# Performance work log

Hardware: AMD Instinct MI355X
Metric: run time of the kernel (lower is better)

The kernel has to match this reference:

```python
import jax, jax.numpy as jnp
import numpy as np

N_HEAD = 16
LORA_RANK = 16
ROPE_BASE = 10000.0


def _rope_cos_sin(T, D, dtype):
    # GPT-NeoX style rotate-half RoPE tables, shape [T, D]
    inv_freq = 1.0 / (ROPE_BASE ** (jnp.arange(0, D, 2, dtype=jnp.float32) / D))
    t = jnp.arange(T, dtype=jnp.float32)
    freqs = t[:, None] * inv_freq[None, :]          # [T, D/2]
    emb = jnp.concatenate([freqs, freqs], axis=-1)   # [T, D]
    return jnp.cos(emb).astype(dtype), jnp.sin(emb).astype(dtype)


def _rotate_half(x):
    x1, x2 = jnp.split(x, 2, axis=-1)
    return jnp.concatenate([-x2, x1], axis=-1)


def _apply_rope(q, k, cos, sin):
    # q,k: [B,H,T,D]; cos,sin: [T,D]
    c = cos[None, None, :, :]
    s = sin[None, None, :, :]
    return q * c + _rotate_half(q) * s, k * c + _rotate_half(k) * s


def setup_inputs() -> dict:
    key = jax.random.key(0)
    ks = jax.random.split(key, 6)
    B, T, C = 4, 1024, 2048
    r = LORA_RANK
    sc = 1.0 / np.sqrt(C)
    return {
        "x": jax.random.normal(ks[0], (B, T, C), jnp.float32),
        "qkvo_delta": jax.random.normal(ks[1], (B, 8 * r, C), jnp.float32) * 0.02,
        "Wq": jax.random.normal(ks[2], (C, C), jnp.float32) * sc,
        "Wk": jax.random.normal(ks[3], (C, C), jnp.float32) * sc,
        "Wv": jax.random.normal(ks[4], (C, C), jnp.float32) * sc,
        "Wo": jax.random.normal(ks[5], (C, C), jnp.float32) * sc,
    }


def reference(x, qkvo_delta, Wq, Wk, Wv, Wo):
    B, T, C = x.shape
    H = N_HEAD
    D = C // H

    # split LoRA deltas: each [B, r, C]
    dqA, dqB, dkA, dkB, dvA, dvB, doA, doB = jnp.split(qkvo_delta, 8, axis=1)

    def merged(W, dB, dA):
        # W [out,in] + dB^T @ dA -> [B, out, in]
        return W[None] + jnp.einsum('bro,bri->boi', dB, dA)

    def proj(inp, Wm):
        # inp @ Wm^T (per-batch merged weight)
        return jnp.einsum('bti,boi->bto', inp, Wm)

    q = proj(x, merged(Wq, dqB, dqA))
    k = proj(x, merged(Wk, dkB, dkA))
    v = proj(x, merged(Wv, dvB, dvA))

    # [B,T,C] -> [B,H,T,D]
    def heads(t):
        return t.reshape(B, T, H, D).transpose(0, 2, 1, 3)

    q, k, v = heads(q), heads(k), heads(v)

    cos, sin = _rope_cos_sin(T, D, x.dtype)
    q, k = _apply_rope(q, k, cos, sin)

    # full (non-causal) SDPA, matching is_causal=False in the source
    scale = 1.0 / np.sqrt(D)
    scores = jnp.einsum('bhtd,bhsd->bhts', q, k) * scale
    attn = jax.nn.softmax(scores, axis=-1)
    y = jnp.einsum('bhts,bhsd->bhtd', attn, v)

    y = y.transpose(0, 2, 1, 3).reshape(B, T, C)
    out = proj(y, merged(Wo, doB, doA))
    return out
```

## Files before the change

kernel.cpp:

```cpp
#include <hip/hip_runtime.h>
#include <cstdint>
#include <cstddef>

typedef __attribute__((ext_vector_type(8))) __bf16 bf8_t;
typedef __attribute__((ext_vector_type(8))) short s8_t;
typedef __attribute__((ext_vector_type(4))) short s4_t;
typedef __attribute__((ext_vector_type(4))) float f4_t;

__device__ __forceinline__ float bf2f(unsigned short h) {
  union { unsigned u; float f; } v; v.u = (unsigned)h << 16; return v.f;
}
__device__ __forceinline__ unsigned short f2bf(float f) {
  union { float f; unsigned u; } v; v.f = f;
  return (unsigned short)((v.u + 0x7FFFu + ((v.u >> 16) & 1u)) >> 16);
}

#define GL16(gp, lp) __builtin_amdgcn_global_load_lds( \
    (__attribute__((address_space(1))) void*)(gp),     \
    (__attribute__((address_space(3))) void*)(lp), 16, 0, 0)

__global__ void k_f32_to_bf16(const float* __restrict__ in,
                              unsigned short* __restrict__ out, int n4) {
  int i = blockIdx.x * blockDim.x + threadIdx.x;
  if (i >= n4) return;
  float4 v = reinterpret_cast<const float4*>(in)[i];
  s4_t o;
  o.x = (short)f2bf(v.x); o.y = (short)f2bf(v.y);
  o.z = (short)f2bf(v.z); o.w = (short)f2bf(v.w);
  reinterpret_cast<s4_t*>(out)[i] = o;
}

struct P4 { const float* in[4]; unsigned short* out[4]; };
__global__ void k_f32_to_bf16_4(P4 a, int n4) {
  int y = blockIdx.y;
  int i = blockIdx.x * blockDim.x + threadIdx.x;
  if (i >= n4) return;
  float4 v = reinterpret_cast<const float4*>(a.in[y])[i];
  s4_t o;
  o.x = (short)f2bf(v.x); o.y = (short)f2bf(v.y);
  o.z = (short)f2bf(v.z); o.w = (short)f2bf(v.w);
  reinterpret_cast<s4_t*>(a.out[y])[i] = o;
}

__global__ void k_rope_table(float* __restrict__ cosT, float* __restrict__ sinT) {
  int t = blockIdx.x, d = threadIdx.x;
  float inv = exp2f(-(float)d * (13.287712379549449f / 64.0f));
  float ang = (float)t * inv;
  cosT[t * 64 + d] = cosf(ang);
  sinT[t * 64 + d] = sinf(ang);
}

__global__ __launch_bounds__(256) void k_lora_mfma(
    const unsigned short* __restrict__ X,
    const unsigned short* __restrict__ dlb,
    float* __restrict__ u, int pstart, int pcount) {
  __shared__ __align__(16) unsigned short Xs[64 * 64];
  __shared__ __align__(16) unsigned short Da[64 * 64];
  const int t = threadIdx.x;
  const int b = blockIdx.y;
  const int m0 = blockIdx.x * 64;
  const int w = t >> 6, lane = t & 63, lr = lane & 15, lg = lane >> 4;
  const int nrow = pcount * 16;
  f4_t acc[4] = {};
  for (int k0 = 0; k0 < 2048; k0 += 64) {
    __syncthreads();
#pragma unroll
    for (int i = 0; i < 2; ++i) {
      int idx = i * 256 + t;
      int row = idx >> 3, c = idx & 7;
      GL16(X + ((size_t)b * 1024 + m0 + row) * 2048 + k0 + ((c ^ (row & 7)) * 8),
           Xs + (size_t)idx * 8);
      int ric = row < nrow ? row : nrow - 1;
      int g = (pstart + (ric >> 4)) * 32 + (ric & 15);
      GL16(dlb + ((size_t)b * 128 + g) * 2048 + k0 + ((c ^ (ric & 7)) * 8),
           Da + (size_t)idx * 8);
    }
    __syncthreads();
#pragma unroll
    for (int kk = 0; kk < 2; ++kk) {
      bf8_t af = *(const bf8_t*)&Xs[(w * 16 + lr) * 64 + (((kk * 4 + lg) ^ (lr & 7)) * 8)];
#pragma unroll
      for (int n = 0; n < 4; ++n) {
        if (n < pcount) {
          bf8_t bfv = *(const bf8_t*)&Da[(n * 16 + lr) * 64 + (((kk * 4 + lg) ^ (lr & 7)) * 8)];
          acc[n] = __builtin_amdgcn_mfma_f32_16x16x32_bf16(af, bfv, acc[n], 0, 0, 0);
        }
      }
    }
  }
#pragma unroll
  for (int n = 0; n < 4; ++n) {
    if (n < pcount) {
#pragma unroll
      for (int j = 0; j < 4; ++j)
        u[(((size_t)b * 4 + pstart + n) * 16 + lr) * 1024 + m0 + w * 16 + lg * 4 + j] = acc[n][j];
    }
  }
}

struct GArgs {
  const unsigned short *Bw0, *Bw1, *Bw2;
  void *o0, *o1, *o2;
  int m0_, m1_, m2_;
  int p0_, p1_, p2_;
};
#define BM 128
#define BN 128
#define BKK 64
__global__ __launch_bounds__(256, 2) void k_gemm(
    const unsigned short* __restrict__ A,
    GArgs ga,
    const float* __restrict__ u,
    const float* __restrict__ dl) {
  constexpr int K = 2048;
  const int z = blockIdx.z;
  const unsigned short* Bw = z == 0 ? ga.Bw0 : (z == 1 ? ga.Bw1 : ga.Bw2);
  void* outv = z == 0 ? ga.o0 : (z == 1 ? ga.o1 : ga.o2);
  const int mode = z == 0 ? ga.m0_ : (z == 1 ? ga.m1_ : ga.m2_);
  const int p = z == 0 ? ga.p0_ : (z == 1 ? ga.p1_ : ga.p2_);
  __shared__ unsigned short As[BM * BKK];
  __shared__ unsigned short Bs[BN * BKK];
  const int t = threadIdx.x;
  const int m0 = blockIdx.y * BM;
  const int n0 = blockIdx.x * BN;
  const int lane = t & 63;
  const int w = t >> 6;
  const int wr = (w >> 1) * 64, wc = (w & 1) * 64;
  const int lr = lane & 15;
  const int lg = lane >> 4;
  const int srow = t >> 3;
  const int sdst = (t & 7) * 8;
  const int ssrc = ((t & 7) ^ (srow & 7)) * 8;
  f4_t acc[4][4] = {};

  for (int k0 = 0; k0 < K; k0 += BKK) {
#pragma unroll
    for (int j = 0; j < 4; ++j) {
      int row = j * 32 + srow;
      GL16(A  + (size_t)(m0 + row) * K + k0 + ssrc, As + row * BKK + sdst);
      GL16(Bw + (size_t)(n0 + row) * K + k0 + ssrc, Bs + row * BKK + sdst);
    }
    __syncthreads();
#pragma unroll
    for (int kk = 0; kk < 2; ++kk) {
      bf8_t af[4], bfr[4];
#pragma unroll
      for (int m = 0; m < 4; ++m) {
        int row_ = wr + m * 16 + lr;
        af[m] = *(const bf8_t*)&As[row_ * BKK + (((kk * 4 + lg) ^ (lr & 7)) * 8)];
      }
#pragma unroll
      for (int n = 0; n < 4; ++n) {
        int row_ = wc + n * 16 + lr;
        bfr[n] = *(const bf8_t*)&Bs[row_ * BKK + (((kk * 4 + lg) ^ (lr & 7)) * 8)];
      }
#pragma unroll
      for (int m = 0; m < 4; ++m)
#pragma unroll
        for (int n = 0; n < 4; ++n)
          acc[m][n] = __builtin_amdgcn_mfma_f32_16x16x32_bf16(af[m], bfr[n], acc[m][n], 0, 0, 0);
    }
    __syncthreads();
  }

  const int b = m0 >> 10;
  const int t0r = m0 & 1023;
  for (int idx = t; idx < 128 * 32; idx += 256) {
    int rr = idx >> 5, r = idx & 31;
    float val = (r < 16) ? u[(((size_t)b * 4 + p) * 16 + r) * 1024 + t0r + rr] : 0.0f;
    As[rr * 32 + r] = f2bf(val);
  }
  for (int idx = t; idx < 128 * 32; idx += 256) {
    int cc = idx >> 5, r = idx & 31;
    float val = (r < 16) ? dl[((size_t)b * 128 + p * 32 + 16 + r) * 2048 + n0 + cc] : 0.0f;
    Bs[cc * 32 + r] = f2bf(val);
  }
  __syncthreads();
  {
    bf8_t af[4], bfr[4];
#pragma unroll
    for (int m = 0; m < 4; ++m)
      af[m] = *(const bf8_t*)&As[(wr + m * 16 + lr) * 32 + lg * 8];
#pragma unroll
    for (int n = 0; n < 4; ++n)
      bfr[n] = *(const bf8_t*)&Bs[(wc + n * 16 + lr) * 32 + lg * 8];
#pragma unroll
    for (int m = 0; m < 4; ++m)
#pragma unroll
      for (int n = 0; n < 4; ++n)
        acc[m][n] = __builtin_amdgcn_mfma_f32_16x16x32_bf16(af[m], bfr[n], acc[m][n], 0, 0, 0);
  }

  unsigned short* out16 = (unsigned short*)outv;
  float* out32 = (float*)outv;
#pragma unroll
  for (int m = 0; m < 4; ++m) {
    int ri = wr + m * 16 + lg * 4;
#pragma unroll
    for (int j = 0; j < 4; ++j) {
      int grow = m0 + ri + j;
      int gb = grow >> 10, gt = grow & 1023;
#pragma unroll
      for (int n = 0; n < 4; ++n) {
        int gcol = n0 + wc + n * 16 + lr;
        float fv = acc[m][n][j];
        if (mode == 0) {
          size_t dst = (((size_t)gb * 16 + (gcol >> 7)) * 1024 + gt) * 128 + (gcol & 127);
          out16[dst] = f2bf(fv);
        } else if (mode == 1) {
          size_t dst = (((size_t)gb * 16 + (gcol >> 7)) * 128 + (gcol & 127)) * 1024 + gt;
          out16[dst] = f2bf(fv);
        } else {
          out32[(size_t)grow * 2048 + gcol] = fv;
        }
      }
    }
  }
}

__global__ void k_rope(unsigned short* __restrict__ X,
                       const float* __restrict__ cosT, const float* __restrict__ sinT) {
  int idx = blockIdx.x * 256 + threadIdx.x;
  int d0 = (idx & 7) * 8;
  int tt = (idx >> 3) & 1023;
  size_t base = (size_t)(idx >> 3) * 128 + d0;
  s8_t a = *(s8_t*)&X[base];
  s8_t bb = *(s8_t*)&X[base + 64];
  float4 c0 = *(const float4*)&cosT[tt * 64 + d0];
  float4 c1 = *(const float4*)&cosT[tt * 64 + d0 + 4];
  float4 sv0 = *(const float4*)&sinT[tt * 64 + d0];
  float4 sv1 = *(const float4*)&sinT[tt * 64 + d0 + 4];
  float cv[8] = {c0.x, c0.y, c0.z, c0.w, c1.x, c1.y, c1.z, c1.w};
  float sw[8] = {sv0.x, sv0.y, sv0.z, sv0.w, sv1.x, sv1.y, sv1.z, sv1.w};
  s8_t ra, rb;
#pragma unroll
  for (int j = 0; j < 8; ++j) {
    float av = bf2f((unsigned short)a[j]);
    float bv = bf2f((unsigned short)bb[j]);
    ra[j] = (short)f2bf(av * cv[j] - bv * sw[j]);
    rb[j] = (short)f2bf(bv * cv[j] + av * sw[j]);
  }
  *(s8_t*)&X[base] = ra;
  *(s8_t*)&X[base + 64] = rb;
}

__global__ __launch_bounds__(512, 4) void k_attn(
    const unsigned short* __restrict__ Qg,
    const unsigned short* __restrict__ Kg,
    const unsigned short* __restrict__ Vt,
    unsigned short* __restrict__ Y) {
  const float scale = 0.08838834764831845f;
  const float L2E = 1.4426950408889634f;
  const int bid = blockIdx.x;
  const int wg = (bid & 7) * 64 + (bid >> 3);
  const int bh = wg >> 3;
  const int b = bh >> 4, h = bh & 15;
  const int t = threadIdx.x;
  const int w = t >> 6, lane = t & 63;
  const int lr = lane & 15, lg = lane >> 4;
  const int q0 = (wg & 7) * 128 + w * 16;
  const unsigned short* Q  = Qg + (size_t)bh * 131072;
  const unsigned short* Kp = Kg + (size_t)bh * 131072;
  const unsigned short* Vp = Vt + (size_t)bh * 131072;
  __shared__ __align__(16) unsigned short Ks[64 * 128];
  __shared__ __align__(16) unsigned short Vs[128 * 64];
  __shared__ __align__(16) unsigned short Ps[8][16 * 72];
  unsigned short* Pw = Ps[w];

  bf8_t qf[4];
#pragma unroll
  for (int kk = 0; kk < 4; ++kk)
    qf[kk] = *(const bf8_t*)&Q[(size_t)(q0 + lr) * 128 + kk * 32 + lg * 8];

  f4_t o[8] = {};
  float m_run = -1e30f, l_run = 0.0f;

  for (int s0 = 0; s0 < 1024; s0 += 64) {
    __syncthreads();
#pragma unroll
    for (int i = 0; i < 2; ++i) {
      int idx = i * 512 + t;
      int s = idx >> 4, c = t & 15;
      GL16(Kp + (size_t)(s0 + s) * 128 + ((c ^ (s & 7)) * 8), Ks + (size_t)idx * 8);
    }
#pragma unroll
    for (int i = 0; i < 2; ++i) {
      int idx = i * 512 + t;
      int d = idx >> 3, c = t & 7;
      GL16(Vp + (size_t)d * 1024 + s0 + ((c ^ (d & 7)) * 8), Vs + (size_t)idx * 8);
    }
    __syncthreads();

    f4_t sf[4];
#pragma unroll
    for (int ss = 0; ss < 4; ++ss) {
      f4_t c = {0.0f, 0.0f, 0.0f, 0.0f};
#pragma unroll
      for (int kk = 0; kk < 4; ++kk) {
        bf8_t kf = *(const bf8_t*)&Ks[(ss * 16 + lr) * 128 + (((kk * 4 + lg) ^ (lr & 7)) * 8)];
        c = __builtin_amdgcn_mfma_f32_16x16x32_bf16(kf, qf[kk], c, 0, 0, 0);
      }
      sf[ss] = c;
    }
    float vmax = -1e30f;
#pragma unroll
    for (int ss = 0; ss < 4; ++ss)
#pragma unroll
      for (int j = 0; j < 4; ++j) vmax = fmaxf(vmax, sf[ss][j]);
    vmax = fmaxf(vmax, __shfl_xor(vmax, 16));
    vmax = fmaxf(vmax, __shfl_xor(vmax, 32));
    float m_new = fmaxf(m_run, vmax * scale);
    float ratio = exp2f((m_run - m_new) * L2E);
    float lsum = 0.0f;
    float ps[4][4];
#pragma unroll
    for (int ss = 0; ss < 4; ++ss)
#pragma unroll
      for (int j = 0; j < 4; ++j) {
        float pv = exp2f((sf[ss][j] * scale - m_new) * L2E);
        ps[ss][j] = pv; lsum += pv;
      }
    lsum += __shfl_xor(lsum, 16);
    lsum += __shfl_xor(lsum, 32);
    l_run = l_run * ratio + lsum;
    m_run = m_new;
    float rq[4];
#pragma unroll
    for (int j = 0; j < 4; ++j) rq[j] = __shfl(ratio, lg * 4 + j);
#pragma unroll
    for (int n = 0; n < 8; ++n)
#pragma unroll
      for (int j = 0; j < 4; ++j) o[n][j] *= rq[j];
#pragma unroll
    for (int ss = 0; ss < 4; ++ss) {
      s4_t pk;
      pk.x = (short)f2bf(ps[ss][0]); pk.y = (short)f2bf(ps[ss][1]);
      pk.z = (short)f2bf(ps[ss][2]); pk.w = (short)f2bf(ps[ss][3]);
      *(s4_t*)&Pw[lr * 72 + ss * 16 + lg * 4] = pk;
    }
    bf8_t pa0 = *(const bf8_t*)&Pw[lr * 72 + lg * 8];
    bf8_t pa1 = *(const bf8_t*)&Pw[lr * 72 + 32 + lg * 8];
#pragma unroll
    for (int n = 0; n < 8; ++n) {
      int d = n * 16 + lr;
      bf8_t v0 = *(const bf8_t*)&Vs[d * 64 + (((0 + lg) ^ (lr & 7)) * 8)];
      bf8_t v1 = *(const bf8_t*)&Vs[d * 64 + (((4 + lg) ^ (lr & 7)) * 8)];
      o[n] = __builtin_amdgcn_mfma_f32_16x16x32_bf16(pa0, v0, o[n], 0, 0, 0);
      o[n] = __builtin_amdgcn_mfma_f32_16x16x32_bf16(pa1, v1, o[n], 0, 0, 0);
    }
  }

  float linv[4];
#pragma unroll
  for (int j = 0; j < 4; ++j) linv[j] = 1.0f / __shfl(l_run, lg * 4 + j);
#pragma unroll
  for (int n = 0; n < 8; ++n)
#pragma unroll
    for (int j = 0; j < 4; ++j) {
      int qg = q0 + lg * 4 + j;
      Y[((size_t)b * 1024 + qg) * 2048 + h * 128 + n * 16 + lr] =
          f2bf(o[n][j] * linv[j]);
    }
}

extern "C" void kernel_launch(void* const* d_in, const int* in_sizes, int n_in,
                              void* d_out, int out_size, void* d_ws, size_t ws_size,
                              hipStream_t stream) {
  const float* x  = (const float*)d_in[0];
  const float* dl = (const float*)d_in[1];
  const float* W[4] = {(const float*)d_in[2], (const float*)d_in[3],
                       (const float*)d_in[4], (const float*)d_in[5]};
  char* ws = (char*)d_ws;
  size_t off = 0;
  auto take = [&](size_t bytes) {
    void* p = ws + off; off += (bytes + 255) & ~(size_t)255; return p;
  };
  unsigned short* xb = (unsigned short*)take(8388608ull * 2);
  unsigned short* Wb[4];
  for (int i = 0; i < 4; ++i) Wb[i] = (unsigned short*)take(4194304ull * 2);
  unsigned short* qb = (unsigned short*)take(8388608ull * 2);
  unsigned short* kb = (unsigned short*)take(8388608ull * 2);
  unsigned short* vT = (unsigned short*)take(8388608ull * 2);
  unsigned short* y  = (unsigned short*)take(8388608ull * 2);
  float* u    = (float*)take(4ull * 4 * 16 * 1024 * 4);
  float* cosT = (float*)take(1024ull * 64 * 4);
  float* sinT = (float*)take(1024ull * 64 * 4);
  unsigned short* dlb = (unsigned short*)take(1048576ull * 2);
  if (off > ws_size) return;

  k_f32_to_bf16<<<8192, 256, 0, stream>>>(x, xb, 2097152);
  P4 pw;
  for (int i = 0; i < 4; ++i) { pw.in[i] = W[i]; pw.out[i] = Wb[i]; }
  k_f32_to_bf16_4<<<dim3(4096, 4), 256, 0, stream>>>(pw, 1048576);
  k_f32_to_bf16<<<1024, 256, 0, stream>>>(dl, dlb, 262144);
  k_rope_table<<<1024, 64, 0, stream>>>(cosT, sinT);
  k_lora_mfma<<<dim3(16, 4), 256, 0, stream>>>(xb, dlb, u, 0, 3);

  GArgs gq;
  gq.Bw0 = Wb[0]; gq.o0 = qb;    gq.m0_ = 0; gq.p0_ = 0;
  gq.Bw1 = Wb[1]; gq.o1 = kb;    gq.m1_ = 0; gq.p1_ = 1;
  gq.Bw2 = Wb[2]; gq.o2 = vT;    gq.m2_ = 1; gq.p2_ = 2;
  k_gemm<<<dim3(16, 32, 3), 256, 0, stream>>>(xb, gq, u, dl);

  k_rope<<<2048, 256, 0, stream>>>(qb, cosT, sinT);
  k_rope<<<2048, 256, 0, stream>>>(kb, cosT, sinT);
  k_attn<<<512, 512, 0, stream>>>(qb, kb, vT, y);
  k_lora_mfma<<<dim3(16, 4), 256, 0, stream>>>(y, dlb, u, 3, 1);

  GArgs go;
  go.Bw0 = Wb[3]; go.o0 = d_out; go.m0_ = 2; go.p0_ = 3;
  go.Bw1 = Wb[3]; go.o1 = d_out; go.m1_ = 2; go.p1_ = 3;
  go.Bw2 = Wb[3]; go.o2 = d_out; go.m2_ = 2; go.p2_ = 3;
  k_gemm<<<dim3(16, 32, 1), 256, 0, stream>>>(y, go, u, dl);
}
```

Before: 360.5 us.

## Fuse conversion and rope launches, split LoRA K, register-prefetch attention tiles

The six f32-to-bf16 conversions become a single launch that picks its segment from the block index, and the two RoPE launches become one. The LoRA projection kernel splits its K dimension over two z-slices for more blocks, and the GEMM epilogue sums the two partial buffers. The attention kernel now prefetches the next K/V tile into registers while computing the current one, instead of loading global-to-LDS directly between two barriers. This trades extra registers and an extra partial-sum read for fewer launches and more overlap of memory with compute.

```diff
diff --git a/kernel.cpp b/kernel.cpp
--- a/kernel.cpp
+++ b/kernel.cpp
@@ -19,27 +19,24 @@
     (__attribute__((address_space(1))) void*)(gp),     \
     (__attribute__((address_space(3))) void*)(lp), 16, 0, 0)
 
-__global__ void k_f32_to_bf16(const float* __restrict__ in,
-                              unsigned short* __restrict__ out, int n4) {
-  int i = blockIdx.x * blockDim.x + threadIdx.x;
-  if (i >= n4) return;
-  float4 v = reinterpret_cast<const float4*>(in)[i];
+struct ConvArgs {
+  const float* src[6];
+  unsigned short* dst[6];
+  int n4[6];
+  int thr[5];
+};
+__global__ void k_conv_all(ConvArgs a) {
+  int blk = blockIdx.x, seg = 0;
+#pragma unroll
+  for (int s = 0; s < 5; ++s) seg += (blk >= a.thr[s]);
+  int base = (seg == 0) ? 0 : a.thr[seg - 1];
+  int i = (blk - base) * 256 + threadIdx.x;
+  if (i >= a.n4[seg]) return;
+  float4 v = reinterpret_cast<const float4*>(a.src[seg])[i];
   s4_t o;
   o.x = (short)f2bf(v.x); o.y = (short)f2bf(v.y);
   o.z = (short)f2bf(v.z); o.w = (short)f2bf(v.w);
-  reinterpret_cast<s4_t*>(out)[i] = o;
-}
-
-struct P4 { const float* in[4]; unsigned short* out[4]; };
-__global__ void k_f32_to_bf16_4(P4 a, int n4) {
-  int y = blockIdx.y;
-  int i = blockIdx.x * blockDim.x + threadIdx.x;
-  if (i >= n4) return;
-  float4 v = reinterpret_cast<const float4*>(a.in[y])[i];
-  s4_t o;
-  o.x = (short)f2bf(v.x); o.y = (short)f2bf(v.y);
-  o.z = (short)f2bf(v.z); o.w = (short)f2bf(v.w);
-  reinterpret_cast<s4_t*>(a.out[y])[i] = o;
+  reinterpret_cast<s4_t*>(a.dst[seg])[i] = o;
 }
 
 __global__ void k_rope_table(float* __restrict__ cosT, float* __restrict__ sinT) {
@@ -50,6 +47,7 @@
   sinT[t * 64 + d] = sinf(ang);
 }
 
+#define UOFF 262144
 __global__ __launch_bounds__(256) void k_lora_mfma(
     const unsigned short* __restrict__ X,
     const unsigned short* __restrict__ dlb,
@@ -58,11 +56,12 @@
   __shared__ __align__(16) unsigned short Da[64 * 64];
   const int t = threadIdx.x;
   const int b = blockIdx.y;
+  const int z = blockIdx.z;
   const int m0 = blockIdx.x * 64;
   const int w = t >> 6, lane = t & 63, lr = lane & 15, lg = lane >> 4;
   const int nrow = pcount * 16;
   f4_t acc[4] = {};
-  for (int k0 = 0; k0 < 2048; k0 += 64) {
+  for (int k0 = z * 1024; k0 < z * 1024 + 1024; k0 += 64) {
     __syncthreads();
 #pragma unroll
     for (int i = 0; i < 2; ++i) {
@@ -93,7 +92,8 @@
     if (n < pcount) {
 #pragma unroll
       for (int j = 0; j < 4; ++j)
-        u[(((size_t)b * 4 + pstart + n) * 16 + lr) * 1024 + m0 + w * 16 + lg * 4 + j] = acc[n][j];
+        u[(size_t)z * UOFF +
+          (((size_t)b * 4 + pstart + n) * 16 + lr) * 1024 + m0 + w * 16 + lg * 4 + j] = acc[n][j];
     }
   }
 }
@@ -167,7 +167,11 @@
   const int t0r = m0 & 1023;
   for (int idx = t; idx < 128 * 32; idx += 256) {
     int rr = idx >> 5, r = idx & 31;
-    float val = (r < 16) ? u[(((size_t)b * 4 + p) * 16 + r) * 1024 + t0r + rr] : 0.0f;
+    float val = 0.0f;
+    if (r < 16) {
+      size_t ub = (((size_t)b * 4 + p) * 16 + r) * 1024 + t0r + rr;
+      val = u[ub] + u[UOFF + ub];
+    }
     As[rr * 32 + r] = f2bf(val);
   }
   for (int idx = t; idx < 128 * 32; idx += 256) {
@@ -218,9 +222,12 @@
   }
 }
 
-__global__ void k_rope(unsigned short* __restrict__ X,
-                       const float* __restrict__ cosT, const float* __restrict__ sinT) {
-  int idx = blockIdx.x * 256 + threadIdx.x;
+__global__ void k_rope2(unsigned short* __restrict__ Xq,
+                        unsigned short* __restrict__ Xk,
+                        const float* __restrict__ cosT, const float* __restrict__ sinT) {
+  int gb = blockIdx.x;
+  unsigned short* X = (gb < 2048) ? Xq : Xk;
+  int idx = (gb & 2047) * 256 + threadIdx.x;
   int d0 = (idx & 7) * 8;
   int tt = (idx >> 3) & 1023;
   size_t base = (size_t)(idx >> 3) * 128 + d0;
@@ -275,21 +282,26 @@
   f4_t o[8] = {};
   float m_run = -1e30f, l_run = 0.0f;
 
+  auto ldK = [&](int s0, int i) {
+    int idx = i * 512 + t, s = idx >> 4, c = t & 15;
+    return *(const s8_t*)&Kp[(size_t)(s0 + s) * 128 + ((c ^ (s & 7)) * 8)];
+  };
+  auto ldV = [&](int s0, int i) {
+    int idx = i * 512 + t, d = idx >> 3, c = t & 7;
+    return *(const s8_t*)&Vp[(size_t)d * 1024 + s0 + ((c ^ (d & 7)) * 8)];
+  };
+  s8_t kr0 = ldK(0, 0), kr1 = ldK(0, 1), vr0 = ldV(0, 0), vr1 = ldV(0, 1);
+
   for (int s0 = 0; s0 < 1024; s0 += 64) {
-    __syncthreads();
-#pragma unroll
-    for (int i = 0; i < 2; ++i) {
-      int idx = i * 512 + t;
-      int s = idx >> 4, c = t & 15;
-      GL16(Kp + (size_t)(s0 + s) * 128 + ((c ^ (s & 7)) * 8), Ks + (size_t)idx * 8);
-    }
-#pragma unroll
-    for (int i = 0; i < 2; ++i) {
-      int idx = i * 512 + t;
-      int d = idx >> 3, c = t & 7;
-      GL16(Vp + (size_t)d * 1024 + s0 + ((c ^ (d & 7)) * 8), Vs + (size_t)idx * 8);
-    }
-    __syncthreads();
+    __builtin_amdgcn_s_barrier();
+    *(s8_t*)&Ks[((size_t)t) * 8]        = kr0;
+    *(s8_t*)&Ks[((size_t)512 + t) * 8]  = kr1;
+    *(s8_t*)&Vs[((size_t)t) * 8]        = vr0;
+    *(s8_t*)&Vs[((size_t)512 + t) * 8]  = vr1;
+    int sn = (s0 < 960) ? s0 + 64 : 0;
+    kr0 = ldK(sn, 0); kr1 = ldK(sn, 1); vr0 = ldV(sn, 0); vr1 = ldV(sn, 1);
+    asm volatile("s_waitcnt lgkmcnt(0)" ::: "memory");
+    __builtin_amdgcn_s_barrier();
 
     f4_t sf[4];
 #pragma unroll
@@ -382,19 +394,20 @@
   unsigned short* kb = (unsigned short*)take(8388608ull * 2);
   unsigned short* vT = (unsigned short*)take(8388608ull * 2);
   unsigned short* y  = (unsigned short*)take(8388608ull * 2);
-  float* u    = (float*)take(4ull * 4 * 16 * 1024 * 4);
+  float* u    = (float*)take(2ull * UOFF * 4);
   float* cosT = (float*)take(1024ull * 64 * 4);
   float* sinT = (float*)take(1024ull * 64 * 4);
   unsigned short* dlb = (unsigned short*)take(1048576ull * 2);
   if (off > ws_size) return;
 
-  k_f32_to_bf16<<<8192, 256, 0, stream>>>(x, xb, 2097152);
-  P4 pw;
-  for (int i = 0; i < 4; ++i) { pw.in[i] = W[i]; pw.out[i] = Wb[i]; }
-  k_f32_to_bf16_4<<<dim3(4096, 4), 256, 0, stream>>>(pw, 1048576);
-  k_f32_to_bf16<<<1024, 256, 0, stream>>>(dl, dlb, 262144);
+  ConvArgs ca;
+  ca.src[0] = x;  ca.dst[0] = xb;  ca.n4[0] = 2097152;
+  for (int i = 0; i < 4; ++i) { ca.src[1 + i] = W[i]; ca.dst[1 + i] = Wb[i]; ca.n4[1 + i] = 1048576; }
+  ca.src[5] = dl; ca.dst[5] = dlb; ca.n4[5] = 262144;
+  ca.thr[0] = 8192; ca.thr[1] = 12288; ca.thr[2] = 16384; ca.thr[3] = 20480; ca.thr[4] = 24576;
+  k_conv_all<<<25600, 256, 0, stream>>>(ca);
   k_rope_table<<<1024, 64, 0, stream>>>(cosT, sinT);
-  k_lora_mfma<<<dim3(16, 4), 256, 0, stream>>>(xb, dlb, u, 0, 3);
+  k_lora_mfma<<<dim3(16, 4, 2), 256, 0, stream>>>(xb, dlb, u, 0, 3);
 
   GArgs gq;
   gq.Bw0 = Wb[0]; gq.o0 = qb;    gq.m0_ = 0; gq.p0_ = 0;
@@ -402,10 +415,9 @@
   gq.Bw2 = Wb[2]; gq.o2 = vT;    gq.m2_ = 1; gq.p2_ = 2;
   k_gemm<<<dim3(16, 32, 3), 256, 0, stream>>>(xb, gq, u, dl);
 
-  k_rope<<<2048, 256, 0, stream>>>(qb, cosT, sinT);
-  k_rope<<<2048, 256, 0, stream>>>(kb, cosT, sinT);
+  k_rope2<<<4096, 256, 0, stream>>>(qb, kb, cosT, sinT);
   k_attn<<<512, 512, 0, stream>>>(qb, kb, vT, y);
-  k_lora_mfma<<<dim3(16, 4), 256, 0, stream>>>(y, dlb, u, 3, 1);
+  k_lora_mfma<<<dim3(16, 4, 2), 256, 0, stream>>>(y, dlb, u, 3, 1);
 
   GArgs go;
   go.Bw0 = Wb[3]; go.o0 = d_out; go.m0_ = 2; go.p0_ = 3;
```

New measurement: 329.9 us. -8.5%, faster.
